# Optimization experiments

Hardware: AMD Instinct MI355X
Metric: run time of the kernel (lower is better)

Reference implementation:

```python
import jax, jax.numpy as jnp
import numpy as np

B, C = 4096, 1          # batch, num_clusters (C forced to 1 by the view in the original)
S = 2048                # sequence_length
AR = 8                  # ar_order
E = 8                   # exogenous_dim
RD = AR + E


def setup_inputs() -> dict:
    key = jax.random.key(0)
    k1, k2, k3 = jax.random.split(key, 3)
    y = jax.random.normal(k1, (B, C, AR + 1), dtype=jnp.float32)
    u = jax.random.normal(k2, (B, C, S + E), dtype=jnp.float32)
    W = jax.random.normal(k3, (C, RD), dtype=jnp.float32) * 0.05
    return {"y": y, "u": u, "W": W}


def reference(y, u, W):
    # Step i (i = 0..S-1, corresponding to t = AR+1+i) reads u[:, :, 1+i : 1+i+E].
    idx = 1 + jnp.arange(S)[:, None] + jnp.arange(E)[None, :]      # [S, E]
    u_win = jnp.transpose(u[:, :, idx], (2, 0, 1, 3))              # [S, B, C, E]

    w = W[0]  # [RD] — valid since num_clusters == 1 (required by original view)

    def step(window, u_t):
        # window: last AR+1 outputs, [B, C, AR+1]; u_t: [B, C, E]
        diffs = window[:, :, 1:] - window[:, :, :-1]               # [B, C, AR]
        reg = jnp.concatenate([diffs, u_t], axis=2)                # [B, C, RD]
        pred = jnp.einsum('bcr,r->bc', reg, w)                     # [B, C]
        new = window[:, :, -1] + pred                              # [B, C]
        new_window = jnp.concatenate([window[:, :, 1:], new[:, :, None]], axis=2)
        return new_window, new

    _, outs = jax.lax.scan(step, y, u_win)                         # outs: [S, B, C]
    out = jnp.concatenate([y, jnp.transpose(outs, (1, 2, 0))], axis=2)  # [B, C, S+AR+1]
    return out
```

## Files before the change

### kernel.cpp

```cpp
#include <hip/hip_runtime.h>

#define B_TOT 4096
#define S_LEN 2048
#define K_CH  64
#define L_CH  32
#define U_ROW 2056
#define O_ROW 2057
#define PROW  2121

__global__ __launch_bounds__(256, 4) void arix_fused(
    const float* __restrict__ y, const float* __restrict__ u,
    const float* __restrict__ W, float* __restrict__ out)
{
    __shared__ float ubuf[4][PROW];
    __shared__ float Msh[6 * 64];
    __shared__ float Csh[6 * 8];
    const int lt = threadIdx.x;
    const int k  = lt & 63;
    const int w  = lt >> 6;
    const int b  = blockIdx.x * 4 + w;

    float wd[8], wu[8];
#pragma unroll
    for (int j = 0; j < 8; ++j) { wd[j] = W[j]; wu[j] = W[8 + j]; }

    const float4* up = (const float4*)(u + (long)b * U_ROW);
    float* ub = ubuf[w];
#pragma unroll
    for (int r = 0; r < 8; ++r) {
        float4 v = up[r * 64 + k];
        const int g = (r * 64 + k) * 4;
        const int idx = g + (g >> 5);
        ub[idx] = v.x; ub[idx + 1] = v.y; ub[idx + 2] = v.z; ub[idx + 3] = v.w;
    }
    if (k < 2) {
        float4 v = up[512 + k];
        const int g = (512 + k) * 4;
        const int idx = g + (g >> 5);
        ub[idx] = v.x; ub[idx + 1] = v.y; ub[idx + 2] = v.z; ub[idx + 3] = v.w;
    }

    const float* yb = y + b * 9;
    float s0[8], x0;
    {
        float yv[9];
#pragma unroll
        for (int i = 0; i < 9; ++i) yv[i] = yb[i];
        if (k < 9) out[(long)b * O_ROW + k] = yv[k];
#pragma unroll
        for (int i = 0; i < 8; ++i) s0[i] = yv[i + 1] - yv[i];
        x0 = yv[8];
    }

    float ua[40];
    {
        const int base = 33 * k;
#pragma unroll
        for (int j = 1; j < 40; ++j) ua[j] = ub[base + j + (j >> 5)];
    }

    float dr[8], x = 0.f;
#pragma unroll
    for (int i = 0; i < 8; ++i) dr[i] = 0.f;
#pragma unroll
    for (int s = 0; s < L_CH; ++s) {
        float acc = wu[0] * ua[s + 1];
#pragma unroll
        for (int j = 1; j < 8; ++j) acc = fmaf(wu[j], ua[s + 1 + j], acc);
#pragma unroll
        for (int j = 0; j < 8; ++j) acc = fmaf(wd[j], dr[j], acc);
#pragma unroll
        for (int j = 0; j < 7; ++j) dr[j] = dr[j + 1];
        dr[7] = acc;
        x += acc;
    }

    if (lt < 8) {
        float tr[8];
#pragma unroll
        for (int i = 0; i < 8; ++i) tr[i] = (i == lt) ? 1.f : 0.f;
        float xs = 0.f;
        for (int t = 0; t < L_CH; ++t) {
            float acc = wd[0] * tr[0];
#pragma unroll
            for (int i = 1; i < 8; ++i) acc = fmaf(wd[i], tr[i], acc);
#pragma unroll
            for (int i = 0; i < 7; ++i) tr[i] = tr[i + 1];
            tr[7] = acc; xs += acc;
        }
#pragma unroll
        for (int i = 0; i < 8; ++i) Msh[i * 8 + lt] = tr[i];
        Csh[lt] = xs;
    }
    __syncthreads();
    for (int l = 1; l < 6; ++l) {
        const float* Mp = Msh + (l - 1) * 64;
        const float* Cp = Csh + (l - 1) * 8;
        float mv = 0.f, cv = 0.f;
        if (lt < 64) {
            const int i = lt >> 3, j = lt & 7;
            float a = 0.f;
#pragma unroll
            for (int m = 0; m < 8; ++m) a = fmaf(Mp[i * 8 + m], Mp[m * 8 + j], a);
            mv = a;
        }
        if (lt < 8) {
            float a = Cp[lt];
#pragma unroll
            for (int i = 0; i < 8; ++i) a = fmaf(Cp[i], Mp[i * 8 + lt], a);
            cv = a;
        }
        __syncthreads();
        if (lt < 64) Msh[l * 64 + lt] = mv;
        if (lt < 8)  Csh[l * 8 + lt] = cv;
        __syncthreads();
    }

    float P[8], Q = x;
#pragma unroll
    for (int i = 0; i < 8; ++i) P[i] = dr[i];

    if (k == 0) {
        float np[8];
#pragma unroll
        for (int i = 0; i < 8; ++i) {
            float a = P[i];
#pragma unroll
            for (int j = 0; j < 8; ++j) a = fmaf(Msh[i * 8 + j], s0[j], a);
            np[i] = a;
        }
        float qa = Q;
#pragma unroll
        for (int j = 0; j < 8; ++j) qa = fmaf(Csh[j], s0[j], qa);
#pragma unroll
        for (int i = 0; i < 8; ++i) P[i] = np[i];
        Q = qa;
    }

#pragma unroll
    for (int l = 0; l < 6; ++l) {
        const int delta = 1 << l;
        float Pl[8], Ql;
#pragma unroll
        for (int i = 0; i < 8; ++i) Pl[i] = __shfl_up(P[i], delta);
        Ql = __shfl_up(Q, delta);
        if (k >= delta) {
            const float* Mp = Msh + l * 64;
            const float* Cp = Csh + l * 8;
            float np[8];
#pragma unroll
            for (int i = 0; i < 8; ++i) {
                float a = P[i];
#pragma unroll
                for (int j = 0; j < 8; ++j) a = fmaf(Mp[i * 8 + j], Pl[j], a);
                np[i] = a;
            }
            float qa = Q + Ql;
#pragma unroll
            for (int j = 0; j < 8; ++j) qa = fmaf(Cp[j], Pl[j], qa);
#pragma unroll
            for (int i = 0; i < 8; ++i) P[i] = np[i];
            Q = qa;
        }
    }

    float Pin[8], Qin;
#pragma unroll
    for (int i = 0; i < 8; ++i) Pin[i] = __shfl_up(P[i], 1);
    Qin = __shfl_up(Q, 1);
    if (k == 0) {
#pragma unroll
        for (int i = 0; i < 8; ++i) Pin[i] = s0[i];
        Qin = 0.f;
    }

#pragma unroll
    for (int i = 0; i < 8; ++i) dr[i] = Pin[i];
    x = x0 + Qin;

    const int obase = 33 * k;
#pragma unroll
    for (int s = 0; s < L_CH; ++s) {
        float acc = wu[0] * ua[s + 1];
#pragma unroll
        for (int j = 1; j < 8; ++j) acc = fmaf(wu[j], ua[s + 1 + j], acc);
#pragma unroll
        for (int j = 0; j < 8; ++j) acc = fmaf(wd[j], dr[j], acc);
#pragma unroll
        for (int j = 0; j < 7; ++j) dr[j] = dr[j + 1];
        dr[7] = acc;
        x += acc;
        ub[obase + s] = x;
    }

    const long orow = (long)b * O_ROW;
#pragma unroll
    for (int r = 0; r < 33; ++r) {
        const int p = r * 64 + k;
        if (p >= 9 && p < O_ROW) {
            const int g = p - 9;
            out[orow + p] = ub[g + (g >> 5)];
        }
    }
}

extern "C" void kernel_launch(void* const* d_in, const int* in_sizes, int n_in,
                              void* d_out, int out_size, void* d_ws, size_t ws_size,
                              hipStream_t stream) {
    const float* y = (const float*)d_in[0];
    const float* u = (const float*)d_in[1];
    const float* W = (const float*)d_in[2];
    float* out = (float*)d_out;

    arix_fused<<<dim3(B_TOT / 4), dim3(256), 0, stream>>>(y, u, W, out);
}
```

Measured before the change: 99.78 us.

## Split each lane's 32-step chunk into two interleaved 16-step subchains

Each lane's 32-step recurrence is split into two independent 16-step halves (A and B) that run interleaved. This breaks the serial FMA dependency chain and adds instruction-level parallelism. The 16-step transfer matrix is composed in shared memory to join half A's state into half B's start, and the scan matrices are rebuilt from that 16-step base. The two-pass structure (zero-state pass, then corrected pass) is kept in a non-unrolled loop to limit code size. The cost is extra matrix-vector work at the join and more register pressure.

```diff
diff --git a/kernel.cpp b/kernel.cpp
--- a/kernel.cpp
+++ b/kernel.cpp
@@ -2,17 +2,37 @@
 
 #define B_TOT 4096
 #define S_LEN 2048
-#define K_CH  64
-#define L_CH  32
 #define U_ROW 2056
 #define O_ROW 2057
 #define PROW  2121
+
+template<int W0>
+__device__ __forceinline__ void step8(const float (&wd)[8], const float (&wu)[8],
+                                      const float (&uw)[32], float (&dr)[8],
+                                      float &x, float (&xo)[8])
+{
+#pragma unroll
+    for (int q = 0; q < 8; ++q) {
+        float acc = wu[0] * uw[W0 + q];
+#pragma unroll
+        for (int m = 1; m < 8; ++m) acc = fmaf(wu[m], uw[W0 + q + m], acc);
+#pragma unroll
+        for (int j = 0; j < 8; ++j) acc = fmaf(wd[j], dr[j], acc);
+#pragma unroll
+        for (int j = 0; j < 7; ++j) dr[j] = dr[j + 1];
+        dr[7] = acc;
+        x += acc;
+        xo[q] = x;
+    }
+}
 
 __global__ __launch_bounds__(256, 4) void arix_fused(
     const float* __restrict__ y, const float* __restrict__ u,
     const float* __restrict__ W, float* __restrict__ out)
 {
     __shared__ float ubuf[4][PROW];
+    __shared__ float Tsh[64];
+    __shared__ float C16sh[8];
     __shared__ float Msh[6 * 64];
     __shared__ float Csh[6 * 8];
     const int lt = threadIdx.x;
@@ -40,47 +60,25 @@
         ub[idx] = v.x; ub[idx + 1] = v.y; ub[idx + 2] = v.z; ub[idx + 3] = v.w;
     }
 
-    const float* yb = y + b * 9;
+    const long orow = (long)b * O_ROW;
     float s0[8], x0;
     {
+        const float* yb = y + b * 9;
         float yv[9];
 #pragma unroll
         for (int i = 0; i < 9; ++i) yv[i] = yb[i];
-        if (k < 9) out[(long)b * O_ROW + k] = yv[k];
+        if (k < 9) out[orow + k] = yv[k];
 #pragma unroll
         for (int i = 0; i < 8; ++i) s0[i] = yv[i + 1] - yv[i];
         x0 = yv[8];
     }
 
-    float ua[40];
-    {
-        const int base = 33 * k;
-#pragma unroll
-        for (int j = 1; j < 40; ++j) ua[j] = ub[base + j + (j >> 5)];
-    }
-
-    float dr[8], x = 0.f;
-#pragma unroll
-    for (int i = 0; i < 8; ++i) dr[i] = 0.f;
-#pragma unroll
-    for (int s = 0; s < L_CH; ++s) {
-        float acc = wu[0] * ua[s + 1];
-#pragma unroll
-        for (int j = 1; j < 8; ++j) acc = fmaf(wu[j], ua[s + 1 + j], acc);
-#pragma unroll
-        for (int j = 0; j < 8; ++j) acc = fmaf(wd[j], dr[j], acc);
-#pragma unroll
-        for (int j = 0; j < 7; ++j) dr[j] = dr[j + 1];
-        dr[7] = acc;
-        x += acc;
-    }
-
     if (lt < 8) {
         float tr[8];
 #pragma unroll
         for (int i = 0; i < 8; ++i) tr[i] = (i == lt) ? 1.f : 0.f;
         float xs = 0.f;
-        for (int t = 0; t < L_CH; ++t) {
+        for (int t = 0; t < 16; ++t) {
             float acc = wd[0] * tr[0];
 #pragma unroll
             for (int i = 1; i < 8; ++i) acc = fmaf(wd[i], tr[i], acc);
@@ -89,117 +87,161 @@
             tr[7] = acc; xs += acc;
         }
 #pragma unroll
-        for (int i = 0; i < 8; ++i) Msh[i * 8 + lt] = tr[i];
-        Csh[lt] = xs;
+        for (int i = 0; i < 8; ++i) Tsh[i * 8 + lt] = tr[i];
+        C16sh[lt] = xs;
     }
     __syncthreads();
-    for (int l = 1; l < 6; ++l) {
-        const float* Mp = Msh + (l - 1) * 64;
-        const float* Cp = Csh + (l - 1) * 8;
-        float mv = 0.f, cv = 0.f;
-        if (lt < 64) {
-            const int i = lt >> 3, j = lt & 7;
-            float a = 0.f;
-#pragma unroll
-            for (int m = 0; m < 8; ++m) a = fmaf(Mp[i * 8 + m], Mp[m * 8 + j], a);
-            mv = a;
-        }
-        if (lt < 8) {
-            float a = Cp[lt];
-#pragma unroll
-            for (int i = 0; i < 8; ++i) a = fmaf(Cp[i], Mp[i * 8 + lt], a);
-            cv = a;
-        }
-        __syncthreads();
-        if (lt < 64) Msh[l * 64 + lt] = mv;
-        if (lt < 8)  Csh[l * 8 + lt] = cv;
-        __syncthreads();
-    }
-
-    float P[8], Q = x;
-#pragma unroll
-    for (int i = 0; i < 8; ++i) P[i] = dr[i];
-
-    if (k == 0) {
-        float np[8];
-#pragma unroll
-        for (int i = 0; i < 8; ++i) {
-            float a = P[i];
-#pragma unroll
-            for (int j = 0; j < 8; ++j) a = fmaf(Msh[i * 8 + j], s0[j], a);
-            np[i] = a;
-        }
-        float qa = Q;
-#pragma unroll
-        for (int j = 0; j < 8; ++j) qa = fmaf(Csh[j], s0[j], qa);
-#pragma unroll
-        for (int i = 0; i < 8; ++i) P[i] = np[i];
-        Q = qa;
-    }
-
-#pragma unroll
-    for (int l = 0; l < 6; ++l) {
-        const int delta = 1 << l;
-        float Pl[8], Ql;
-#pragma unroll
-        for (int i = 0; i < 8; ++i) Pl[i] = __shfl_up(P[i], delta);
-        Ql = __shfl_up(Q, delta);
-        if (k >= delta) {
-            const float* Mp = Msh + l * 64;
-            const float* Cp = Csh + l * 8;
-            float np[8];
+    {
+        const float* Mp = Tsh; const float* Cp = C16sh;
+#pragma unroll 1
+        for (int l = 0; l < 6; ++l) {
+            float mv = 0.f, cv = 0.f;
+            if (lt < 64) {
+                const int i = lt >> 3, j = lt & 7;
+#pragma unroll
+                for (int m = 0; m < 8; ++m) mv = fmaf(Mp[i * 8 + m], Mp[m * 8 + j], mv);
+            }
+            if (lt < 8) {
+                cv = Cp[lt];
+#pragma unroll
+                for (int i = 0; i < 8; ++i) cv = fmaf(Cp[i], Mp[i * 8 + lt], cv);
+            }
+            __syncthreads();
+            if (lt < 64) Msh[l * 64 + lt] = mv;
+            if (lt < 8)  Csh[l * 8 + lt] = cv;
+            __syncthreads();
+            Mp = Msh + l * 64; Cp = Csh + l * 8;
+        }
+    }
+
+    const int ubase = 33 * k;
+    float drA[8], drB[8], PA[8], xA = 0.f, xB = 0.f, QA = 0.f;
+#pragma unroll
+    for (int i = 0; i < 8; ++i) { drA[i] = 0.f; drB[i] = 0.f; }
+
+#pragma unroll 1
+    for (int p = 0; p < 2; ++p) {
+        if (p) {
+            QA = xA;
+#pragma unroll
+            for (int i = 0; i < 8; ++i) PA[i] = drA[i];
+            float P[8], Q;
 #pragma unroll
             for (int i = 0; i < 8; ++i) {
-                float a = P[i];
-#pragma unroll
-                for (int j = 0; j < 8; ++j) a = fmaf(Mp[i * 8 + j], Pl[j], a);
-                np[i] = a;
-            }
-            float qa = Q + Ql;
-#pragma unroll
-            for (int j = 0; j < 8; ++j) qa = fmaf(Cp[j], Pl[j], qa);
-#pragma unroll
-            for (int i = 0; i < 8; ++i) P[i] = np[i];
-            Q = qa;
-        }
-    }
-
-    float Pin[8], Qin;
-#pragma unroll
-    for (int i = 0; i < 8; ++i) Pin[i] = __shfl_up(P[i], 1);
-    Qin = __shfl_up(Q, 1);
-    if (k == 0) {
-#pragma unroll
-        for (int i = 0; i < 8; ++i) Pin[i] = s0[i];
-        Qin = 0.f;
-    }
-
-#pragma unroll
-    for (int i = 0; i < 8; ++i) dr[i] = Pin[i];
-    x = x0 + Qin;
-
-    const int obase = 33 * k;
-#pragma unroll
-    for (int s = 0; s < L_CH; ++s) {
-        float acc = wu[0] * ua[s + 1];
-#pragma unroll
-        for (int j = 1; j < 8; ++j) acc = fmaf(wu[j], ua[s + 1 + j], acc);
-#pragma unroll
-        for (int j = 0; j < 8; ++j) acc = fmaf(wd[j], dr[j], acc);
-#pragma unroll
-        for (int j = 0; j < 7; ++j) dr[j] = dr[j + 1];
-        dr[7] = acc;
-        x += acc;
-        ub[obase + s] = x;
-    }
-
-    const long orow = (long)b * O_ROW;
-#pragma unroll
+                float a = drB[i];
+#pragma unroll
+                for (int j = 0; j < 8; ++j) a = fmaf(Tsh[i * 8 + j], PA[j], a);
+                P[i] = a;
+            }
+            {
+                float qa = QA + xB;
+#pragma unroll
+                for (int j = 0; j < 8; ++j) qa = fmaf(C16sh[j], PA[j], qa);
+                Q = qa;
+            }
+            if (k == 0) {
+                float np[8];
+#pragma unroll
+                for (int i = 0; i < 8; ++i) {
+                    float a = P[i];
+#pragma unroll
+                    for (int j = 0; j < 8; ++j) a = fmaf(Msh[i * 8 + j], s0[j], a);
+                    np[i] = a;
+                }
+                float qa = Q;
+#pragma unroll
+                for (int j = 0; j < 8; ++j) qa = fmaf(Csh[j], s0[j], qa);
+#pragma unroll
+                for (int i = 0; i < 8; ++i) P[i] = np[i];
+                Q = qa;
+            }
+#pragma unroll 1
+            for (int l = 0; l < 6; ++l) {
+                const int delta = 1 << l;
+                float Pl[8], Ql;
+#pragma unroll
+                for (int i = 0; i < 8; ++i) Pl[i] = __shfl_up(P[i], delta);
+                Ql = __shfl_up(Q, delta);
+                if (k >= delta) {
+                    const float* Mp = Msh + l * 64;
+                    const float* Cp = Csh + l * 8;
+                    float np[8];
+#pragma unroll
+                    for (int i = 0; i < 8; ++i) {
+                        float a = P[i];
+#pragma unroll
+                        for (int j = 0; j < 8; ++j) a = fmaf(Mp[i * 8 + j], Pl[j], a);
+                        np[i] = a;
+                    }
+                    float qa = Q + Ql;
+#pragma unroll
+                    for (int j = 0; j < 8; ++j) qa = fmaf(Cp[j], Pl[j], qa);
+#pragma unroll
+                    for (int i = 0; i < 8; ++i) P[i] = np[i];
+                    Q = qa;
+                }
+            }
+            float Pin[8], Qin;
+#pragma unroll
+            for (int i = 0; i < 8; ++i) Pin[i] = __shfl_up(P[i], 1);
+            Qin = __shfl_up(Q, 1);
+            if (k == 0) {
+#pragma unroll
+                for (int i = 0; i < 8; ++i) Pin[i] = s0[i];
+                Qin = 0.f;
+            }
+#pragma unroll
+            for (int i = 0; i < 8; ++i) drA[i] = Pin[i];
+            xA = x0 + Qin;
+#pragma unroll
+            for (int i = 0; i < 8; ++i) {
+                float a = PA[i];
+#pragma unroll
+                for (int j = 0; j < 8; ++j) a = fmaf(Tsh[i * 8 + j], Pin[j], a);
+                drB[i] = a;
+            }
+            {
+                float qa = xA + QA;
+#pragma unroll
+                for (int j = 0; j < 8; ++j) qa = fmaf(C16sh[j], Pin[j], qa);
+                xB = qa;
+            }
+        }
+
+        float uw[32];
+#pragma unroll
+        for (int c = 0; c < 32; ++c) uw[c] = ub[ubase + (c + 1) + ((c + 1) >> 5)];
+
+        float xoA0[8], xoB0[8], xoA1[8], xoB1[8];
+        step8<0>(wd, wu, uw, drA, xA, xoA0);
+        step8<16>(wd, wu, uw, drB, xB, xoB0);
+
+#pragma unroll
+        for (int c = 0; c < 24; ++c) uw[c] = uw[c + 8];
+#pragma unroll
+        for (int c = 0; c < 8; ++c) uw[24 + c] = ub[ubase + 34 + c];
+
+        step8<0>(wd, wu, uw, drA, xA, xoA1);
+        step8<16>(wd, wu, uw, drB, xB, xoB1);
+
+        asm volatile("" ::: "memory");
+        if (p) {
+#pragma unroll
+            for (int q = 0; q < 8; ++q) {
+                ub[ubase + q]      = xoA0[q];
+                ub[ubase + 8 + q]  = xoA1[q];
+                ub[ubase + 16 + q] = xoB0[q];
+                ub[ubase + 24 + q] = xoB1[q];
+            }
+        }
+    }
+
+#pragma unroll 4
     for (int r = 0; r < 33; ++r) {
-        const int p = r * 64 + k;
-        if (p >= 9 && p < O_ROW) {
-            const int g = p - 9;
-            out[orow + p] = ub[g + (g >> 5)];
+        const int pz = r * 64 + k;
+        if (pz >= 9 && pz < O_ROW) {
+            const int g = pz - 9;
+            out[orow + pz] = ub[g + (g >> 5)];
         }
     }
 }
```

Result: slower. 104.5 us (+4.7%).
